# Performance work log

Hardware: AMD Instinct MI355X
Metric: run time of the kernel (lower is better)

The kernel has to match this reference:

```python
import jax, jax.numpy as jnp
import numpy as np

N = 100_000      # nodes
E = 500_000      # bonds
DN = 128         # dim_node_embedding
DB = 64          # dim_bond_embedding
NTOK = 4         # num_bond_token
DIN = 2 * DN + 2 * DB  # 384
LEAKY = 0.001
LN_EPS = 1e-5
DIST_MAX = 20.0
STEP = 0.5


def _lrelu(v):
    return jnp.where(v >= 0, v, LEAKY * v)


def _layernorm(v, w, b):
    m = v.mean(-1, keepdims=True)
    var = ((v - m) ** 2).mean(-1, keepdims=True)
    return (v - m) / jnp.sqrt(var + LN_EPS) * w + b


def setup_inputs() -> dict:
    key = jax.random.key(0)
    ks = jax.random.split(key, 20)
    x = jax.random.normal(ks[0], (N, 3), dtype=jnp.float32) * 3.0
    pos = jax.random.normal(ks[1], (N, 3), dtype=jnp.float32)
    node_embedding = jax.random.normal(ks[2], (N, DN), dtype=jnp.float32)
    i0 = jax.random.randint(ks[3], (E,), 0, N)
    off = jax.random.randint(ks[4], (E,), 1, N)  # nonzero -> no self-bonds
    bond_index = jnp.stack([i0, (i0 + off) % N], axis=1).astype(jnp.int32)
    bond_types = jax.random.randint(ks[5], (E,), 0, NTOK).astype(jnp.int32)
    s = 0.02
    params = dict(
        bond_emb=jax.random.normal(ks[6], (NTOK, DB), dtype=jnp.float32),
        W0=jax.random.normal(ks[7], (DIN, DN), dtype=jnp.float32) * s,
        b0=jnp.zeros((DN,), jnp.float32),
        W1=jax.random.normal(ks[8], (DN, DN), dtype=jnp.float32) * s,
        b1=jnp.zeros((DN,), jnp.float32),
        ln1_w=jnp.ones((DN,), jnp.float32),
        ln1_b=jnp.zeros((DN,), jnp.float32),
        W2=jax.random.normal(ks[9], (DN, DN), dtype=jnp.float32) * s,
        b2=jnp.zeros((DN,), jnp.float32),
        ln2_w=jnp.ones((DN,), jnp.float32),
        ln2_b=jnp.zeros((DN,), jnp.float32),
        Wo=jax.random.normal(ks[10], (DN, 2), dtype=jnp.float32) * s,
        bo=jnp.zeros((2,), jnp.float32),
    )
    return dict(x=x, pos=pos, node_embedding=node_embedding,
                bond_index=bond_index, bond_types=bond_types, **params)


def reference(x, pos, node_embedding, bond_index, bond_types,
              bond_emb, W0, b0, W1, b1, ln1_w, ln1_b,
              W2, b2, ln2_w, ln2_b, Wo, bo):
    i = bond_index[:, 0]
    j = bond_index[:, 1]

    # ---- BondLength geometry ----
    diff = x[i] - x[j]                                   # [E,3]
    dist = jnp.linalg.norm(diff, axis=-1, keepdims=True)  # [E,1]
    u = diff / dist                                       # [E,3] unit j->i? (i-j)/d
    direction = jnp.stack([u, -u], axis=-1)               # [E,3,2]

    # ---- Smearing (gaussian RBF + overflow bin, normalized) ----
    offset = jnp.linspace(0.0, DIST_MAX, DB - 1, dtype=jnp.float32)  # [63]
    delta = DIST_MAX / (DB - 2)
    coeff = -0.5 / (delta * delta)
    rbf = jnp.exp(coeff * (dist - offset) ** 2)            # [E,63]
    ovf = (dist >= DIST_MAX).astype(x.dtype)               # [E,1]
    smear = jnp.concatenate([rbf, ovf], axis=-1)           # [E,64]
    smear = smear / smear.sum(axis=-1, keepdims=True)

    # ---- Edge MLP (LeakyMLP, num_layer=2, dim_end=2) ----
    feat = jnp.concatenate(
        [node_embedding[i], node_embedding[j], bond_emb[bond_types], smear],
        axis=-1)                                           # [E,384]
    h = _lrelu(feat @ W0 + b0)
    h = _lrelu(_layernorm(h @ W1 + b1, ln1_w, ln1_b))
    h = _lrelu(_layernorm(h @ W2 + b2, ln2_w, ln2_b))
    force = h @ Wo + bo                                    # [E,2]

    # ---- position update (scatter-add) ----
    update = force[:, None, :] * direction                 # [E,3,2]
    pos = pos.at[i].add(STEP * update[..., 0])
    pos = pos.at[j].add(STEP * update[..., 1])
    return pos
```

## Files before the change

kernel.cpp:

```cpp
#include <hip/hip_runtime.h>
#include <stdint.h>

#define N_EDGES 500000
#define N_NODES 100000
#define PREP_NG 2
#define TBINS 5120

typedef __attribute__((ext_vector_type(8))) short short8;
typedef __attribute__((ext_vector_type(4))) float floatx4;
typedef __attribute__((ext_vector_type(2))) float f32x2;

__device__ __forceinline__ uint16_t f2bf(float f) {
  union { float f; uint32_t u; } cv; cv.f = f;
  uint32_t u = cv.u;
  return (uint16_t)((u + 0x7FFFu + ((u >> 16) & 1u)) >> 16);
}
__device__ __forceinline__ uint32_t pk2bf(float lo, float hi) {
  return __builtin_amdgcn_perm(__float_as_uint(hi), __float_as_uint(lo), 0x07060302u);
}
__device__ __forceinline__ uint16_t bftrunc(float f) {
  return (uint16_t)(__float_as_uint(f) >> 16);
}
__device__ __forceinline__ float lrelu(float v) { return fmaxf(v, 0.001f * v); }

__device__ __forceinline__ f32x2 unpk2(uint32_t u) {
  return (f32x2){ __uint_as_float(u << 16), __uint_as_float(u & 0xFFFF0000u) };
}
__device__ __forceinline__ uint32_t comp2n(uint32_t a, uint32_t b, uint32_t t) {
  f32x2 r = unpk2(a) + unpk2(b) + unpk2(t);
  f32x2 rl = r * 0.001f;
  return pk2bf(fmaxf(r.x, rl.x), fmaxf(r.y, rl.y));
}
__device__ __forceinline__ floatx4 lrelu4(floatx4 v) {
  floatx4 w = v * 0.001f;
  v.x = fmaxf(v.x, w.x); v.y = fmaxf(v.y, w.y);
  v.z = fmaxf(v.z, w.z); v.w = fmaxf(v.w, w.w);
  return v;
}

__global__ void prep0_kernel(const float* __restrict__ W0, const float* __restrict__ b0,
                             const float* __restrict__ W1, const float* __restrict__ W2,
                             const float* __restrict__ bemb,
                             uint16_t* __restrict__ w0ab, uint16_t* __restrict__ w1f,
                             uint16_t* __restrict__ w2f, float* __restrict__ be0f,
                             const float* __restrict__ pos, float* __restrict__ out, int npos) {
  int id = blockIdx.x * 256 + threadIdx.x;
  if (id < 32768) {
    int f = id;
    int j = f & 7, lane = (f >> 3) & 63, ntt = (f >> 9) & 15, ks = f >> 13;
    int k = ks * 32 + (lane >> 4) * 8 + j;
    int row = (ntt < 8) ? k : (128 + k);
    int col = (ntt & 7) * 16 + (lane & 15);
    w0ab[f] = f2bf(W0[row * 128 + col]);
  } else if (id < 49152) {
    int f = id - 32768;
    int j = f & 7, lane = (f >> 3) & 63, nt = (f >> 9) & 7, ks = f >> 12;
    int k = ks * 32 + (lane >> 4) * 8 + j;
    w1f[f] = f2bf(W1[k * 128 + nt * 16 + (lane & 15)]);
  } else if (id < 65536) {
    int f = id - 49152;
    int j = f & 7, lane = (f >> 3) & 63, nt = (f >> 9) & 7, ks = f >> 12;
    int k = ks * 32 + (lane >> 4) * 8 + j;
    w2f[f] = f2bf(W2[k * 128 + nt * 16 + (lane & 15)]);
  } else if (id < 66048) {
    int t = id - 65536; int ty = t >> 7, n = t & 127;
    float s = b0[n];
    for (int kk = 0; kk < 64; ++kk) s += bemb[ty * 64 + kk] * W0[(256 + kk) * 128 + n];
    be0f[t] = s;
  } else if (id - 66048 < npos) {
    out[id - 66048] = pos[id - 66048];
  }
}

__global__ __attribute__((amdgpu_flat_work_group_size(256, 256)))
void prep_tp_kernel(const float* __restrict__ W0, const float* __restrict__ be0f,
                    uint16_t* __restrict__ T,
                    const float* __restrict__ nemb, const uint16_t* __restrict__ w0ab,
                    uint16_t* __restrict__ Pa, uint16_t* __restrict__ Pb) {
  __shared__ __align__(16) uint16_t aLds[4 * PREP_NG * 16 * 136];
  __shared__ __align__(16) uint16_t sS[4][16][72];
  __shared__ float rbf[64];
  const int tid = threadIdx.x;

  if (blockIdx.x < TBINS) {
    int b = blockIdx.x;
    float dist = (float)b * (1.0f / 128.0f);
    const float delta = 20.0f / 62.0f;
    const float coeff = -0.5f / (delta * delta);
    if (tid < 64) {
      float v;
      if (tid < 63) { float d = dist - (float)tid * delta; v = __expf(coeff * d * d); }
      else v = (dist >= 20.0f) ? 1.0f : 0.0f;
      rbf[tid] = v;
    }
    __syncthreads();
    float sum = 0.0f;
    for (int k = 0; k < 64; ++k) sum += rbf[k];
    float rs = 1.0f / sum;
    for (int o = tid; o < 512; o += 256) {
      int ty = o >> 7, n = o & 127;
      float s = be0f[ty * 128 + n];
      for (int k = 0; k < 64; ++k) s += rbf[k] * rs * W0[(320 + k) * 128 + n];
      T[((size_t)(ty * TBINS + b)) * 128 + n] = f2bf(s);
    }
    return;
  }

  const int pblk = blockIdx.x - TBINS;
  const int lane = tid & 63;
  const int wave = tid >> 6;
  const int n15 = lane & 15;
  const int quad = lane >> 4;
  uint16_t* myA = aLds + wave * (PREP_NG * 16 * 136);
  const int base = pblk * (64 * PREP_NG) + wave * (16 * PREP_NG);

  {
    const int le = lane >> 2, sub = lane & 3;
#pragma unroll
    for (int it = 0; it < PREP_NG; ++it) {
      int r = base + it * 16 + le; if (r >= N_NODES) r = N_NODES - 1;
      const float4* src = (const float4*)(nemb + (size_t)r * 128);
#pragma unroll
      for (int g = 0; g < 4; ++g) {
        float4 a = src[sub * 8 + g * 2], b = src[sub * 8 + g * 2 + 1];
        uint4 pk;
        pk.x = pk2bf(a.x, a.y); pk.y = pk2bf(a.z, a.w);
        pk.z = pk2bf(b.x, b.y); pk.w = pk2bf(b.z, b.w);
        *(uint4*)(myA + (it * 16 + le) * 136 + sub * 32 + g * 8) = pk;
      }
    }
  }

  const short8* wfv = (const short8*)w0ab + lane;
  const int srow = lane >> 2, sch = lane & 3;
#pragma unroll
  for (int q = 0; q < 4; ++q) {
    short8 bfr[16];
#pragma unroll
    for (int ks = 0; ks < 4; ++ks)
#pragma unroll
      for (int nq = 0; nq < 4; ++nq)
        bfr[ks * 4 + nq] = wfv[(ks * 16 + q * 4 + nq) * 64];
    uint16_t* dst = (q < 2) ? Pa : Pb;
    const int cbase = (q & 1) * 64;
#pragma unroll
    for (int it = 0; it < PREP_NG; ++it) {
      floatx4 acc[4];
#pragma unroll
      for (int nq = 0; nq < 4; ++nq) acc[nq] = (floatx4){0.f, 0.f, 0.f, 0.f};
#pragma unroll
      for (int ks = 0; ks < 4; ++ks) {
        short8 a = *(const short8*)(myA + (it * 16 + n15) * 136 + ks * 32 + quad * 8);
#pragma unroll
        for (int nq = 0; nq < 4; ++nq)
          acc[nq] = __builtin_amdgcn_mfma_f32_16x16x32_bf16(a, bfr[ks * 4 + nq], acc[nq], 0, 0, 0);
      }
#pragma unroll
      for (int nq = 0; nq < 4; ++nq)
#pragma unroll
        for (int r = 0; r < 4; ++r)
          sS[wave][quad * 4 + r][nq * 16 + n15] = bftrunc(acc[nq][r]);
      int grow = base + it * 16 + srow;
      if (grow < N_NODES) {
        uint16_t* drow = dst + (size_t)grow * 128 + cbase;
#pragma unroll
        for (int h = 0; h < 2; ++h)
          *(uint4*)(drow + (h * 4 + sch) * 8) =
              *(const uint4*)&sS[wave][srow][(h * 4 + sch) * 8];
      }
    }
  }
}

__device__ __forceinline__ void gemm_g(const uint16_t* __restrict__ wf, const uint16_t* aRow,
                                       int lane, floatx4* acc) {
  short8 a[4];
#pragma unroll
  for (int ks = 0; ks < 4; ++ks) a[ks] = *(const short8*)(aRow + ks * 32);
  const short8* wv = (const short8*)wf + lane;
#pragma unroll
  for (int ks = 0; ks < 4; ++ks)
#pragma unroll
    for (int nt = 0; nt < 8; ++nt)
      acc[nt] = __builtin_amdgcn_mfma_f32_16x16x32_bf16(a[ks], wv[(ks * 8 + nt) * 64], acc[nt], 0, 0, 0);
}

__global__ __attribute__((amdgpu_flat_work_group_size(256, 256), amdgpu_waves_per_eu(4)))
void bond_mlp_kernel(const float* __restrict__ x,
                     const int* __restrict__ bidx, const int* __restrict__ btyp,
                     const uint16_t* __restrict__ Pa, const uint16_t* __restrict__ Pb,
                     const uint16_t* __restrict__ Tt, const uint16_t* __restrict__ w1f,
                     const uint16_t* __restrict__ w2f,
                     const float* __restrict__ b1, const float* __restrict__ ln1w,
                     const float* __restrict__ ln1b,
                     const float* __restrict__ b2, const float* __restrict__ ln2w,
                     const float* __restrict__ ln2b,
                     const float* __restrict__ Wo, const float* __restrict__ bo,
                     float* __restrict__ out) {
  __shared__ __align__(16) uint16_t hA_all[4 * 16 * 136];
  __shared__ float u_lds[64][3];
  __shared__ int ij_lds[64][2];

  const int tid = threadIdx.x;
  const int lane = tid & 63;
  const int wave = tid >> 6;
  const int n15 = lane & 15;
  const int quad = lane >> 4;

  uint16_t* hA = hA_all + wave * (16 * 136);

  {
    const int le = lane >> 2, sub = lane & 3;
    const int gr = wave * 16 + le;
    const int ge = blockIdx.x * 64 + gr;
    const bool valid = ge < N_EDGES;
    int vi = 0, vj = 0, bt = 0;
    if (valid) {
      int2 ij = *(const int2*)(bidx + 2 * ge);
      vi = ij.x; vj = ij.y;
      bt = btyp[ge];
    }
    float dx, dy, dz;
    if (valid) {
      dx = x[3 * vi]     - x[3 * vj];
      dy = x[3 * vi + 1] - x[3 * vj + 1];
      dz = x[3 * vi + 2] - x[3 * vj + 2];
    } else { dx = 1.0f; dy = 0.0f; dz = 0.0f; }
    float dist = sqrtf(dx * dx + dy * dy + dz * dz);
    float rinv = 1.0f / dist;
    if (sub == 0) {
      u_lds[gr][0] = dx * rinv; u_lds[gr][1] = dy * rinv; u_lds[gr][2] = dz * rinv;
      ij_lds[gr][0] = vi; ij_lds[gr][1] = vj;
    }
    int bi = (int)(fminf(dist, 39.9f) * 128.0f + 0.5f);
    const uint4* pa = (const uint4*)(Pa + (size_t)vi * 128 + sub * 32);
    const uint4* pb = (const uint4*)(Pb + (size_t)vj * 128 + sub * 32);
    const uint4* tp = (const uint4*)(Tt + ((size_t)(bt * TBINS + bi)) * 128 + sub * 32);
#pragma unroll
    for (int g = 0; g < 4; ++g) {
      uint4 av = pa[g], bv = pb[g], tv = tp[g];
      uint4 pk;
      pk.x = comp2n(av.x, bv.x, tv.x);
      pk.y = comp2n(av.y, bv.y, tv.y);
      pk.z = comp2n(av.z, bv.z, tv.z);
      pk.w = comp2n(av.w, bv.w, tv.w);
      *(uint4*)(hA + le * 136 + sub * 32 + g * 8) = pk;
    }
  }

  const uint16_t* aRow = hA + n15 * 136 + quad * 8;

  floatx4 acc[8];
#pragma unroll
  for (int nt = 0; nt < 8; ++nt) acc[nt] = (floatx4){0.f, 0.f, 0.f, 0.f};
  gemm_g(w1f, aRow, lane, acc);

  {
    float bv[8], wv[8], bb[8];
#pragma unroll
    for (int nt = 0; nt < 8; ++nt) {
      int col = nt * 16 + n15;
      bv[nt] = b1[col]; wv[nt] = ln1w[col]; bb[nt] = ln1b[col];
    }
    floatx4 s4 = {0.f, 0.f, 0.f, 0.f}, q4 = {0.f, 0.f, 0.f, 0.f};
#pragma unroll
    for (int nt = 0; nt < 8; ++nt) { floatx4 v = acc[nt] + bv[nt]; s4 += v; q4 += v * v; }
#pragma unroll
    for (int m = 1; m <= 8; m <<= 1) {
#pragma unroll
      for (int c = 0; c < 4; ++c) { s4[c] += __shfl_xor(s4[c], m); q4[c] += __shfl_xor(q4[c], m); }
    }
    floatx4 mean = s4 * (1.0f / 128.0f);
    floatx4 var = q4 * (1.0f / 128.0f) - mean * mean;
    floatx4 rstd;
    rstd.x = rsqrtf(var.x + 1e-5f); rstd.y = rsqrtf(var.y + 1e-5f);
    rstd.z = rsqrtf(var.z + 1e-5f); rstd.w = rsqrtf(var.w + 1e-5f);
#pragma unroll
    for (int nt = 0; nt < 8; ++nt) {
      floatx4 v = acc[nt] + bv[nt];
      floatx4 vn = lrelu4((v - mean) * (rstd * wv[nt]) + bb[nt]);
#pragma unroll
      for (int r = 0; r < 4; ++r)
        hA[(quad * 4 + r) * 136 + nt * 16 + n15] = bftrunc(vn[r]);
    }
  }

#pragma unroll
  for (int nt = 0; nt < 8; ++nt) acc[nt] = (floatx4){0.f, 0.f, 0.f, 0.f};
  gemm_g(w2f, aRow, lane, acc);

  {
    float bv[8], wv[8], bb[8], wo0[8], wo1[8];
#pragma unroll
    for (int nt = 0; nt < 8; ++nt) {
      int col = nt * 16 + n15;
      bv[nt] = b2[col]; wv[nt] = ln2w[col]; bb[nt] = ln2b[col];
      wo0[nt] = Wo[2 * col]; wo1[nt] = Wo[2 * col + 1];
    }
    floatx4 s4 = {0.f, 0.f, 0.f, 0.f}, q4 = {0.f, 0.f, 0.f, 0.f};
#pragma unroll
    for (int nt = 0; nt < 8; ++nt) { floatx4 v = acc[nt] + bv[nt]; s4 += v; q4 += v * v; }
#pragma unroll
    for (int m = 1; m <= 8; m <<= 1) {
#pragma unroll
      for (int c = 0; c < 4; ++c) { s4[c] += __shfl_xor(s4[c], m); q4[c] += __shfl_xor(q4[c], m); }
    }
    floatx4 mean = s4 * (1.0f / 128.0f);
    floatx4 var = q4 * (1.0f / 128.0f) - mean * mean;
    floatx4 rstd;
    rstd.x = rsqrtf(var.x + 1e-5f); rstd.y = rsqrtf(var.y + 1e-5f);
    rstd.z = rsqrtf(var.z + 1e-5f); rstd.w = rsqrtf(var.w + 1e-5f);
    floatx4 f0 = {0.f, 0.f, 0.f, 0.f}, f1 = {0.f, 0.f, 0.f, 0.f};
#pragma unroll
    for (int nt = 0; nt < 8; ++nt) {
      floatx4 v = acc[nt] + bv[nt];
      floatx4 vn = lrelu4((v - mean) * (rstd * wv[nt]) + bb[nt]);
      f0 += vn * wo0[nt];
      f1 += vn * wo1[nt];
    }
#pragma unroll
    for (int m = 1; m <= 8; m <<= 1) {
#pragma unroll
      for (int c = 0; c < 4; ++c) { f0[c] += __shfl_xor(f0[c], m); f1[c] += __shfl_xor(f1[c], m); }
    }
    if (n15 < 4) {
      int gr = wave * 16 + quad * 4 + n15;
      int ge2 = blockIdx.x * 64 + gr;
      if (ge2 < N_EDGES) {
        float F0 = (n15 == 0) ? f0.x : (n15 == 1) ? f0.y : (n15 == 2) ? f0.z : f0.w;
        float F1 = (n15 == 0) ? f1.x : (n15 == 1) ? f1.y : (n15 == 2) ? f1.z : f1.w;
        F0 += bo[0]; F1 += bo[1];
        float ux = u_lds[gr][0], uy = u_lds[gr][1], uz = u_lds[gr][2];
        int ii = ij_lds[gr][0], jj = ij_lds[gr][1];
        float c0 = 0.5f * F0;
        float c1 = -0.5f * F1;
        atomicAdd(out + 3 * ii,     c0 * ux);
        atomicAdd(out + 3 * ii + 1, c0 * uy);
        atomicAdd(out + 3 * ii + 2, c0 * uz);
        atomicAdd(out + 3 * jj,     c1 * ux);
        atomicAdd(out + 3 * jj + 1, c1 * uy);
        atomicAdd(out + 3 * jj + 2, c1 * uz);
      }
    }
  }
}

extern "C" void kernel_launch(void* const* d_in, const int* in_sizes, int n_in,
                              void* d_out, int out_size, void* d_ws, size_t ws_size,
                              hipStream_t stream) {
  const float* x    = (const float*)d_in[0];
  const float* pos  = (const float*)d_in[1];
  const float* nemb = (const float*)d_in[2];
  const int*   bidx = (const int*)d_in[3];
  const int*   btyp = (const int*)d_in[4];
  const float* bemb = (const float*)d_in[5];
  const float* W0   = (const float*)d_in[6];
  const float* b0   = (const float*)d_in[7];
  const float* W1   = (const float*)d_in[8];
  const float* b1   = (const float*)d_in[9];
  const float* ln1w = (const float*)d_in[10];
  const float* ln1b = (const float*)d_in[11];
  const float* W2   = (const float*)d_in[12];
  const float* b2   = (const float*)d_in[13];
  const float* ln2w = (const float*)d_in[14];
  const float* ln2b = (const float*)d_in[15];
  const float* Wo   = (const float*)d_in[16];
  const float* bo   = (const float*)d_in[17];
  float* out = (float*)d_out;

  uint16_t* w0ab = (uint16_t*)d_ws;
  uint16_t* w1f  = w0ab + 32768;
  uint16_t* w2f  = w1f + 16384;
  float*    be0f = (float*)(w2f + 16384);
  uint16_t* Tt   = (uint16_t*)(be0f + 512);
  uint16_t* Pa   = Tt + (size_t)4 * TBINS * 128;
  uint16_t* Pb   = Pa + (size_t)N_NODES * 128;

  const int nblkP = (N_NODES + 64 * PREP_NG - 1) / (64 * PREP_NG);

  prep0_kernel<<<(66048 + out_size + 255) / 256, 256, 0, stream>>>(
      W0, b0, W1, W2, bemb, w0ab, w1f, w2f, be0f, pos, out, out_size);
  prep_tp_kernel<<<TBINS + nblkP, 256, 0, stream>>>(
      W0, be0f, Tt, nemb, w0ab, Pa, Pb);
  bond_mlp_kernel<<<(N_EDGES + 63) / 64, 256, 0, stream>>>(
      x, bidx, btyp, Pa, Pb, Tt, w1f, w2f,
      b1, ln1w, ln1b, b2, ln2w, ln2b, Wo, bo, out);
}
```

Baseline: 352.6 us.

## Coarsen smear table with linear interpolation and precompute per-edge geometry records

Shrinks the precomputed distance-to-layer0 table from 5120 to 1280 bins per bond type and linearly interpolates between adjacent rows in the bond kernel. This cuts prep_tp work and table footprint. Edge geometry (unit direction plus a packed row index and interpolation weight) is now computed once in prep0 into a float4 record per edge. The bond kernel reads that record instead of gathering x and recomputing the distance, which also removes the LDS staging. The cost is an extra table row read per edge, a 16-byte record written and read per edge, and an interpolation error that differs from the finer nearest-bin lookup.

```diff
diff --git a/kernel.cpp b/kernel.cpp
--- a/kernel.cpp
+++ b/kernel.cpp
@@ -4,7 +4,7 @@
 #define N_EDGES 500000
 #define N_NODES 100000
 #define PREP_NG 2
-#define TBINS 5120
+#define TBINS 1280
 
 typedef __attribute__((ext_vector_type(8))) short short8;
 typedef __attribute__((ext_vector_type(4))) float floatx4;
@@ -26,8 +26,11 @@
 __device__ __forceinline__ f32x2 unpk2(uint32_t u) {
   return (f32x2){ __uint_as_float(u << 16), __uint_as_float(u & 0xFFFF0000u) };
 }
-__device__ __forceinline__ uint32_t comp2n(uint32_t a, uint32_t b, uint32_t t) {
-  f32x2 r = unpk2(a) + unpk2(b) + unpk2(t);
+__device__ __forceinline__ uint32_t comp2(uint32_t a, uint32_t b, uint32_t t0, uint32_t t1,
+                                          f32x2 w2) {
+  f32x2 p  = unpk2(a) + unpk2(b);
+  f32x2 v0 = unpk2(t0), v1 = unpk2(t1);
+  f32x2 r  = p + (v0 + w2 * (v1 - v0));
   f32x2 rl = r * 0.001f;
   return pk2bf(fmaxf(r.x, rl.x), fmaxf(r.y, rl.y));
 }
@@ -41,8 +44,11 @@
 __global__ void prep0_kernel(const float* __restrict__ W0, const float* __restrict__ b0,
                              const float* __restrict__ W1, const float* __restrict__ W2,
                              const float* __restrict__ bemb,
+                             const float* __restrict__ x, const int* __restrict__ bidx,
+                             const int* __restrict__ btyp,
                              uint16_t* __restrict__ w0ab, uint16_t* __restrict__ w1f,
                              uint16_t* __restrict__ w2f, float* __restrict__ be0f,
+                             float4* __restrict__ erec,
                              const float* __restrict__ pos, float* __restrict__ out, int npos) {
   int id = blockIdx.x * 256 + threadIdx.x;
   if (id < 32768) {
@@ -69,6 +75,26 @@
     be0f[t] = s;
   } else if (id - 66048 < npos) {
     out[id - 66048] = pos[id - 66048];
+  } else {
+    int e = id - 66048 - npos;
+    if (e < N_EDGES) {
+      int2 ij = *(const int2*)(bidx + 2 * e);
+      int bt = btyp[e];
+      float xi0 = x[3 * ij.x], xi1 = x[3 * ij.x + 1], xi2 = x[3 * ij.x + 2];
+      float xj0 = x[3 * ij.y], xj1 = x[3 * ij.y + 1], xj2 = x[3 * ij.y + 2];
+      float dx = xi0 - xj0, dy = xi1 - xj1, dz = xi2 - xj2;
+      float dist = sqrtf(dx * dx + dy * dy + dz * dz);
+      float rinv = 1.0f / dist;
+      float fb = fminf(dist, 39.5f) * 32.0f;
+      int bi = (int)fb;
+      uint32_t wq = (uint32_t)((fb - (float)bi) * 65536.0f);
+      if (wq > 65535u) wq = 65535u;
+      uint32_t pk = (uint32_t)(bt * TBINS + bi) | (wq << 16);
+      float4 r;
+      r.x = dx * rinv; r.y = dy * rinv; r.z = dz * rinv;
+      r.w = __uint_as_float(pk);
+      erec[e] = r;
+    }
   }
 }
 
@@ -84,7 +110,7 @@
 
   if (blockIdx.x < TBINS) {
     int b = blockIdx.x;
-    float dist = (float)b * (1.0f / 128.0f);
+    float dist = (float)b * (1.0f / 32.0f);
     const float delta = 20.0f / 62.0f;
     const float coeff = -0.5f / (delta * delta);
     if (tid < 64) {
@@ -186,8 +212,8 @@
 }
 
 __global__ __attribute__((amdgpu_flat_work_group_size(256, 256), amdgpu_waves_per_eu(4)))
-void bond_mlp_kernel(const float* __restrict__ x,
-                     const int* __restrict__ bidx, const int* __restrict__ btyp,
+void bond_mlp_kernel(const int* __restrict__ bidx,
+                     const float4* __restrict__ erec,
                      const uint16_t* __restrict__ Pa, const uint16_t* __restrict__ Pb,
                      const uint16_t* __restrict__ Tt, const uint16_t* __restrict__ w1f,
                      const uint16_t* __restrict__ w2f,
@@ -198,8 +224,6 @@
                      const float* __restrict__ Wo, const float* __restrict__ bo,
                      float* __restrict__ out) {
   __shared__ __align__(16) uint16_t hA_all[4 * 16 * 136];
-  __shared__ float u_lds[64][3];
-  __shared__ int ij_lds[64][2];
 
   const int tid = threadIdx.x;
   const int lane = tid & 63;
@@ -211,40 +235,32 @@
 
   {
     const int le = lane >> 2, sub = lane & 3;
-    const int gr = wave * 16 + le;
-    const int ge = blockIdx.x * 64 + gr;
+    const int ge = blockIdx.x * 64 + wave * 16 + le;
     const bool valid = ge < N_EDGES;
-    int vi = 0, vj = 0, bt = 0;
+    int vi = 0, vj = 0;
+    uint32_t pk = 0;
     if (valid) {
       int2 ij = *(const int2*)(bidx + 2 * ge);
       vi = ij.x; vj = ij.y;
-      bt = btyp[ge];
-    }
-    float dx, dy, dz;
-    if (valid) {
-      dx = x[3 * vi]     - x[3 * vj];
-      dy = x[3 * vi + 1] - x[3 * vj + 1];
-      dz = x[3 * vi + 2] - x[3 * vj + 2];
-    } else { dx = 1.0f; dy = 0.0f; dz = 0.0f; }
-    float dist = sqrtf(dx * dx + dy * dy + dz * dz);
-    float rinv = 1.0f / dist;
-    if (sub == 0) {
-      u_lds[gr][0] = dx * rinv; u_lds[gr][1] = dy * rinv; u_lds[gr][2] = dz * rinv;
-      ij_lds[gr][0] = vi; ij_lds[gr][1] = vj;
-    }
-    int bi = (int)(fminf(dist, 39.9f) * 128.0f + 0.5f);
+      pk = __float_as_uint(erec[ge].w);
+    }
+    int row = pk & 0xFFFFu;
+    float w = (float)(pk >> 16) * (1.0f / 65536.0f);
+    f32x2 w2 = {w, w};
     const uint4* pa = (const uint4*)(Pa + (size_t)vi * 128 + sub * 32);
     const uint4* pb = (const uint4*)(Pb + (size_t)vj * 128 + sub * 32);
-    const uint4* tp = (const uint4*)(Tt + ((size_t)(bt * TBINS + bi)) * 128 + sub * 32);
+    const uint16_t* trow = Tt + (size_t)row * 128 + sub * 32;
+    const uint4* t0p = (const uint4*)trow;
+    const uint4* t1p = (const uint4*)(trow + 128);
 #pragma unroll
     for (int g = 0; g < 4; ++g) {
-      uint4 av = pa[g], bv = pb[g], tv = tp[g];
-      uint4 pk;
-      pk.x = comp2n(av.x, bv.x, tv.x);
-      pk.y = comp2n(av.y, bv.y, tv.y);
-      pk.z = comp2n(av.z, bv.z, tv.z);
-      pk.w = comp2n(av.w, bv.w, tv.w);
-      *(uint4*)(hA + le * 136 + sub * 32 + g * 8) = pk;
+      uint4 av = pa[g], bv = pb[g], t0 = t0p[g], t1 = t1p[g];
+      uint4 opk;
+      opk.x = comp2(av.x, bv.x, t0.x, t1.x, w2);
+      opk.y = comp2(av.y, bv.y, t0.y, t1.y, w2);
+      opk.z = comp2(av.z, bv.z, t0.z, t1.z, w2);
+      opk.w = comp2(av.w, bv.w, t0.w, t1.w, w2);
+      *(uint4*)(hA + le * 136 + sub * 32 + g * 8) = opk;
     }
   }
 
@@ -324,22 +340,21 @@
       for (int c = 0; c < 4; ++c) { f0[c] += __shfl_xor(f0[c], m); f1[c] += __shfl_xor(f1[c], m); }
     }
     if (n15 < 4) {
-      int gr = wave * 16 + quad * 4 + n15;
-      int ge2 = blockIdx.x * 64 + gr;
+      int ge2 = blockIdx.x * 64 + wave * 16 + quad * 4 + n15;
       if (ge2 < N_EDGES) {
         float F0 = (n15 == 0) ? f0.x : (n15 == 1) ? f0.y : (n15 == 2) ? f0.z : f0.w;
         float F1 = (n15 == 0) ? f1.x : (n15 == 1) ? f1.y : (n15 == 2) ? f1.z : f1.w;
         F0 += bo[0]; F1 += bo[1];
-        float ux = u_lds[gr][0], uy = u_lds[gr][1], uz = u_lds[gr][2];
-        int ii = ij_lds[gr][0], jj = ij_lds[gr][1];
+        float4 rec = erec[ge2];
+        int2 ij = *(const int2*)(bidx + 2 * ge2);
         float c0 = 0.5f * F0;
         float c1 = -0.5f * F1;
-        atomicAdd(out + 3 * ii,     c0 * ux);
-        atomicAdd(out + 3 * ii + 1, c0 * uy);
-        atomicAdd(out + 3 * ii + 2, c0 * uz);
-        atomicAdd(out + 3 * jj,     c1 * ux);
-        atomicAdd(out + 3 * jj + 1, c1 * uy);
-        atomicAdd(out + 3 * jj + 2, c1 * uz);
+        atomicAdd(out + 3 * ij.x,     c0 * rec.x);
+        atomicAdd(out + 3 * ij.x + 1, c0 * rec.y);
+        atomicAdd(out + 3 * ij.x + 2, c0 * rec.z);
+        atomicAdd(out + 3 * ij.y,     c1 * rec.x);
+        atomicAdd(out + 3 * ij.y + 1, c1 * rec.y);
+        atomicAdd(out + 3 * ij.y + 2, c1 * rec.z);
       }
     }
   }
@@ -375,14 +390,17 @@
   uint16_t* Tt   = (uint16_t*)(be0f + 512);
   uint16_t* Pa   = Tt + (size_t)4 * TBINS * 128;
   uint16_t* Pb   = Pa + (size_t)N_NODES * 128;
+  float4*   erec = (float4*)(Pb + (size_t)N_NODES * 128);
 
   const int nblkP = (N_NODES + 64 * PREP_NG - 1) / (64 * PREP_NG);
-
-  prep0_kernel<<<(66048 + out_size + 255) / 256, 256, 0, stream>>>(
-      W0, b0, W1, W2, bemb, w0ab, w1f, w2f, be0f, pos, out, out_size);
+  const int n0 = 66048 + out_size + N_EDGES;
+
+  prep0_kernel<<<(n0 + 255) / 256, 256, 0, stream>>>(
+      W0, b0, W1, W2, bemb, x, bidx, btyp,
+      w0ab, w1f, w2f, be0f, erec, pos, out, out_size);
   prep_tp_kernel<<<TBINS + nblkP, 256, 0, stream>>>(
       W0, be0f, Tt, nemb, w0ab, Pa, Pb);
   bond_mlp_kernel<<<(N_EDGES + 63) / 64, 256, 0, stream>>>(
-      x, bidx, btyp, Pa, Pb, Tt, w1f, w2f,
+      bidx, erec, Pa, Pb, Tt, w1f, w2f,
       b1, ln1w, ln1b, b2, ln2w, ln2b, Wo, bo, out);
 }
```

Result: no change. 354.7 us (+0.6%).
